# Performance work log

Measured on AMD Instinct MI355X. Metric: run time of the kernel, lower is better.

## Reference

```python
import math
import jax, jax.numpy as jnp
from jax import lax
import numpy as np

E = 16        # num experts
K = 2         # top_k
CF = 1.25     # capacity factor


def setup_inputs() -> dict:
    key = jax.random.key(0)
    k0, k1, k2, k3, k4 = jax.random.split(key, 5)
    B, S, D, H = 2, 2048, 1024, 1024
    scale = 0.02
    return {
        "x": jax.random.normal(k0, (B, S, D), dtype=jnp.float32),
        "router_w": jax.random.normal(k1, (D, E), dtype=jnp.float32) * scale,
        "gate_w": jax.random.normal(k2, (E, D, H), dtype=jnp.float32) * scale,
        "up_w": jax.random.normal(k3, (E, D, H), dtype=jnp.float32) * scale,
        "down_w": jax.random.normal(k4, (E, H, D), dtype=jnp.float32) * scale,
    }


def reference(x, router_w, gate_w, up_w, down_w):
    B, S, D = x.shape
    xf = x.reshape(-1, D)                     # [T, D]
    T = B * S
    capacity = max(1, math.ceil(T * K / E * CF))   # static python int
    Cbuf = K * capacity                       # per-expert buffer (per-column capacity x K)

    # ---- router: softmax over experts, then top-k (weights = top-k probs) ----
    logits = xf @ router_w                    # [T, E]
    probs = jax.nn.softmax(logits, axis=-1)
    w, idx = lax.top_k(probs, K)              # [T, K] each

    # ---- capacity drop: per k-column, per expert, keep first `capacity` tokens ----
    oh = jax.nn.one_hot(idx, E, dtype=w.dtype)            # [T, K, E]
    rank = jnp.cumsum(oh, axis=0) - oh                     # exclusive rank per (k, e)
    myrank = jnp.sum(rank * oh, axis=-1)                   # [T, K]
    keep = myrank < capacity
    w = jnp.where(keep, w, 0.0)

    # ---- dispatch: scatter kept assignments into [E, Cbuf] slots ----
    flat_e = idx.reshape(-1)                               # [A], A = T*K (row-major: token-major)
    flat_w = w.reshape(-1)
    keep_f = keep.reshape(-1)
    tok = jnp.repeat(jnp.arange(T, dtype=jnp.int32), K)    # [A]
    ohk = jax.nn.one_hot(flat_e, E, dtype=jnp.int32) * keep_f[:, None].astype(jnp.int32)
    pos = jnp.cumsum(ohk, axis=0) - ohk                    # exclusive rank among kept per expert
    slot = jnp.sum(pos * ohk, axis=-1)                     # [A], < Cbuf for kept
    e_idx = jnp.where(keep_f, flat_e, E)                   # dropped -> dummy expert row E

    dispatch = jnp.full((E + 1, Cbuf), T, dtype=jnp.int32).at[e_idx, slot].set(tok)
    wbuf = jnp.zeros((E + 1, Cbuf), dtype=w.dtype).at[e_idx, slot].set(flat_w)
    dispatch = dispatch[:E]
    wbuf = wbuf[:E]

    x_pad = jnp.concatenate([xf, jnp.zeros((1, D), xf.dtype)], axis=0)  # sentinel row
    xe = x_pad[dispatch]                                   # [E, Cbuf, D]

    # ---- grouped SwiGLU expert GEMMs ----
    gate = jnp.einsum('ecd,edh->ech', xe, gate_w)
    up = jnp.einsum('ecd,edh->ech', xe, up_w)
    hidden = jax.nn.silu(gate) * up
    out = jnp.einsum('ech,ehd->ecd', hidden, down_w)       # [E, Cbuf, D]
    out = out * wbuf[:, :, None]

    # ---- combine: scatter-add back to tokens ----
    combined = jnp.zeros((T + 1, D), dtype=xf.dtype).at[dispatch.reshape(-1)].add(out.reshape(-1, D))
    return combined[:T].reshape(B, S, D)
```

## Files before the change

kernel.cpp:

```cpp
#include <hip/hip_runtime.h>
#include <math.h>

#define T_TOK 4096
#define DIM   1024
#define HID   1024
#define NE    16
#define CAP   640
#define CBUF  1280
#define BM 128
#define BN 128
#define BK 32
#define MAXTILE 160

typedef __attribute__((ext_vector_type(8))) short short8;
typedef __attribute__((ext_vector_type(4))) float f32x4;

static __device__ __forceinline__ unsigned short f2bf(float f) {
    unsigned int u = __float_as_uint(f);
    u += 0x7fff + ((u >> 16) & 1);
    return (unsigned short)(u >> 16);
}

static __device__ __forceinline__ void async16(const void* g, void* l) {
    __builtin_amdgcn_global_load_lds((const __attribute__((address_space(1))) void*)g,
                                     (__attribute__((address_space(3))) void*)l, 16, 0, 0);
}

__global__ void convert_x_k(const float* __restrict__ x, unsigned short* __restrict__ xb) {
    int i = blockIdx.x * blockDim.x + threadIdx.x;
    int base = i * 4;
    int row = base >> 10;
    ushort4 o;
    if (row < T_TOK) {
        float4 v = *(const float4*)(x + base);
        o.x = f2bf(v.x); o.y = f2bf(v.y); o.z = f2bf(v.z); o.w = f2bf(v.w);
    } else {
        o.x = 0; o.y = 0; o.z = 0; o.w = 0;
    }
    *(ushort4*)(xb + base) = o;
}

#define TSP 68
__global__ void transpose_cvt_k(const float* __restrict__ W0, const float* __restrict__ W1,
                                const float* __restrict__ W2,
                                unsigned short* __restrict__ T0, unsigned short* __restrict__ T1,
                                unsigned short* __restrict__ T2) {
    __shared__ unsigned short s[64 * TSP];
    int zz = blockIdx.z;
    int which = zz >> 4, e = zz & 15;
    const float* W = (which == 0) ? W0 : (which == 1) ? W1 : W2;
    unsigned short* T = (which == 0) ? T0 : (which == 1) ? T1 : T2;
    const float* Wp = W + (size_t)e * DIM * HID;
    unsigned short* Tp = T + (size_t)e * DIM * HID;
    int k0 = blockIdx.y * 64, n0 = blockIdx.x * 64;
    int tid = threadIdx.x;
    int tx = tid & 15, ty = tid >> 4;
    #pragma unroll
    for (int i = 0; i < 4; ++i) {
        int k = ty + i * 16;
        float4 v = *(const float4*)(Wp + (size_t)(k0 + k) * 1024 + n0 + tx * 4);
        int nb = tx * 4;
        s[(nb + 0) * TSP + k] = f2bf(v.x);
        s[(nb + 1) * TSP + k] = f2bf(v.y);
        s[(nb + 2) * TSP + k] = f2bf(v.z);
        s[(nb + 3) * TSP + k] = f2bf(v.w);
    }
    __syncthreads();
    int n = tid >> 2, cseg = (tid & 3) * 16;
    union { ushort4 h[4]; uint4 q[2]; } u;
    #pragma unroll
    for (int j = 0; j < 4; ++j)
        u.h[j] = *(ushort4*)&s[n * TSP + cseg + 4 * j];
    unsigned short* orow = Tp + (size_t)(n0 + n) * 1024 + k0 + cseg;
    *(uint4*)(orow + 0) = u.q[0];
    *(uint4*)(orow + 8) = u.q[1];
}

__global__ void router_k(const float* __restrict__ x, const float* __restrict__ rw,
                         int* __restrict__ route_e, float* __restrict__ route_w) {
    int t = blockIdx.x;
    int lane = threadIdx.x;
    const float* xr = x + (size_t)t * DIM + lane * 16;
    float4 xv0 = *(const float4*)(xr + 0);
    float4 xv1 = *(const float4*)(xr + 4);
    float4 xv2 = *(const float4*)(xr + 8);
    float4 xv3 = *(const float4*)(xr + 12);
    float xl[16] = {xv0.x, xv0.y, xv0.z, xv0.w, xv1.x, xv1.y, xv1.z, xv1.w,
                    xv2.x, xv2.y, xv2.z, xv2.w, xv3.x, xv3.y, xv3.z, xv3.w};
    float p[16];
    #pragma unroll
    for (int e = 0; e < 16; ++e) p[e] = 0.f;
    #pragma unroll
    for (int j = 0; j < 16; ++j) {
        const float4* rp = (const float4*)(rw + (size_t)(lane * 16 + j) * 16);
        float4 r0 = rp[0], r1 = rp[1], r2 = rp[2], r3 = rp[3];
        float xv = xl[j];
        p[0]  += xv * r0.x; p[1]  += xv * r0.y; p[2]  += xv * r0.z; p[3]  += xv * r0.w;
        p[4]  += xv * r1.x; p[5]  += xv * r1.y; p[6]  += xv * r1.z; p[7]  += xv * r1.w;
        p[8]  += xv * r2.x; p[9]  += xv * r2.y; p[10] += xv * r2.z; p[11] += xv * r2.w;
        p[12] += xv * r3.x; p[13] += xv * r3.y; p[14] += xv * r3.z; p[15] += xv * r3.w;
    }
    #pragma unroll
    for (int off = 32; off > 0; off >>= 1) {
        #pragma unroll
        for (int e = 0; e < 16; ++e) p[e] += __shfl_xor(p[e], off);
    }
    if (lane == 0) {
        float m = p[0];
        #pragma unroll
        for (int e = 1; e < 16; ++e) m = fmaxf(m, p[e]);
        float s = 0.f;
        #pragma unroll
        for (int e = 0; e < 16; ++e) s = s + __expf(p[e] - m);
        float v0 = -1e30f, v1 = -1e30f; int i0 = 0, i1 = 0;
        #pragma unroll
        for (int e = 0; e < 16; ++e) {
            float v = p[e];
            if (v > v0)      { v1 = v0; i1 = i0; v0 = v; i0 = e; }
            else if (v > v1) { v1 = v;  i1 = e; }
        }
        route_e[t*2+0] = i0;  route_e[t*2+1] = i1;
        route_w[t*2+0] = __expf(v0 - m) / s;
        route_w[t*2+1] = __expf(v1 - m) / s;
    }
}

__global__ __launch_bounds__(1024)
void build_dispatch_k(const int* __restrict__ route_e, const float* __restrict__ route_w,
                      int* __restrict__ disp, int* __restrict__ smap, int* __restrict__ tmeta) {
    __shared__ unsigned char eidx[2 * T_TOK];
    __shared__ unsigned char keepf[2 * T_TOK];
    __shared__ int totals[NE];
    int tid = threadIdx.x;
    int wv = tid >> 6, lane = tid & 63;

    {
        int4 a = ((const int4*)route_e)[tid * 2];
        int4 b = ((const int4*)route_e)[tid * 2 + 1];
        unsigned int lo = (a.x & 0xff) | ((a.y & 0xff) << 8) | ((a.z & 0xff) << 16) | ((a.w & 0xff) << 24);
        unsigned int hi = (b.x & 0xff) | ((b.y & 0xff) << 8) | ((b.z & 0xff) << 16) | ((b.w & 0xff) << 24);
        uint2 pk; pk.x = lo; pk.y = hi;
        *(uint2*)(eidx + tid * 8) = pk;
    }
    for (int i = tid; i < 2 * T_TOK; i += 1024) smap[i] = -1;
    __syncthreads();

    unsigned long long below = (lane == 0) ? 0ull : ((~0ull) >> (64 - lane));
    #pragma unroll
    for (int s = 0; s < 2; ++s) {
        int st = wv + s * 16;
        int e = st >> 1, k = st & 1;
        int run = 0;
        for (int base = 0; base < T_TOK; base += 64) {
            int t = base + lane;
            int hit = (eidx[t * 2 + k] == e);
            unsigned long long m = __ballot(hit);
            int rank = run + __popcll(m & below);
            if (hit) keepf[t * 2 + k] = (rank < CAP) ? 1 : 0;
            run += __popcll(m);
        }
    }
    __syncthreads();

    {
        int e = wv;
        int run = 0;
        for (int base = 0; base < 2 * T_TOK; base += 64) {
            int f = base + lane;
            int hit = (eidx[f] == e) && keepf[f];
            unsigned long long m = __ballot(hit);
            int slot = run + __popcll(m & below);
            if (hit) {
                disp[e * CBUF + slot] = f >> 1;
                smap[f] = e * CBUF + slot;
            }
            run += __popcll(m);
        }
        if (lane == 0) totals[e] = run;
    }
    __syncthreads();

    for (int i = tid; i < NE * CBUF; i += 1024) {
        int e = i / CBUF, s = i - e * CBUF;
        if (s >= totals[e]) disp[i] = T_TOK;
    }

    if (tid == 0) {
        int n = 0;
        for (int e = 0; e < NE; ++e) {
            int ntl = (totals[e] + BM - 1) / BM;
            for (int m = 0; m < ntl; ++m) { tmeta[4 + n] = (e << 8) | m; ++n; }
        }
        tmeta[0] = n;
    }
}

__global__ __launch_bounds__(256, 2)
void gemm1_k(const unsigned short* __restrict__ xb, const unsigned short* __restrict__ gt,
             const unsigned short* __restrict__ ut, const int* __restrict__ disp,
             const int* __restrict__ tmeta, unsigned short* __restrict__ hidden) {
    int slot = blockIdx.y;
    if (slot >= tmeta[0]) return;
    int pk = tmeta[4 + slot];
    int e = pk >> 8, mt = pk & 255;
    int m0 = mt * BM, n0 = blockIdx.x * BN;

    __shared__ unsigned short As[2 * BM * BK];
    __shared__ unsigned short Bg[2 * BN * BK];
    __shared__ unsigned short Bu[2 * BN * BK];
    __shared__ int tok[BM];
    int tid = threadIdx.x;
    if (tid < BM) tok[tid] = disp[e * CBUF + m0 + tid];
    __syncthreads();

    int lane = tid & 63, w = tid >> 6;
    int cg = (lane & 3) ^ ((lane >> 3) & 3);
    int rl = lane >> 2;
    int rA0 = w * 32 + rl, rA1 = rA0 + 16;
    const unsigned short* srcA0 = xb + (size_t)tok[rA0] * DIM + cg * 8;
    const unsigned short* srcA1 = xb + (size_t)tok[rA1] * DIM + cg * 8;
    const unsigned short* srcG0 = gt + ((size_t)e * HID + n0 + rA0) * DIM + cg * 8;
    const unsigned short* srcG1 = gt + ((size_t)e * HID + n0 + rA1) * DIM + cg * 8;
    const unsigned short* srcU0 = ut + ((size_t)e * HID + n0 + rA0) * DIM + cg * 8;
    const unsigned short* srcU1 = ut + ((size_t)e * HID + n0 + rA1) * DIM + cg * 8;
    unsigned short* dA0 = As + (w * 32) * BK;
    unsigned short* dA1 = As + (w * 32 + 16) * BK;
    unsigned short* dG0 = Bg + (w * 32) * BK;
    unsigned short* dG1 = Bg + (w * 32 + 16) * BK;
    unsigned short* dU0 = Bu + (w * 32) * BK;
    unsigned short* dU1 = Bu + (w * 32 + 16) * BK;

    int wm = w >> 1, wn = w & 1;
    int quad = lane >> 4, ln = lane & 15;
    int swq = quad ^ ((ln >> 1) & 3);

    f32x4 zero4 = {0.f, 0.f, 0.f, 0.f};
    f32x4 accg[4][4], accu[4][4];
    #pragma unroll
    for (int i = 0; i < 4; ++i)
        #pragma unroll
        for (int j = 0; j < 4; ++j) { accg[i][j] = zero4; accu[i][j] = zero4; }

    async16(srcA0, dA0); async16(srcA1, dA1);
    async16(srcG0, dG0); async16(srcG1, dG1);
    async16(srcU0, dU0); async16(srcU1, dU1);

    for (int k0 = 0; k0 < DIM; k0 += BK) {
        int cur = (k0 >> 5) & 1;
        asm volatile("s_waitcnt vmcnt(0)\n\ts_barrier" ::: "memory");
        if (k0 + BK < DIM) {
            int nx = cur ^ 1, nk = k0 + BK;
            async16(srcA0 + nk, dA0 + nx * (BM * BK));
            async16(srcA1 + nk, dA1 + nx * (BM * BK));
            async16(srcG0 + nk, dG0 + nx * (BN * BK));
            async16(srcG1 + nk, dG1 + nx * (BN * BK));
            async16(srcU0 + nk, dU0 + nx * (BN * BK));
            async16(srcU1 + nk, dU1 + nx * (BN * BK));
        }
        const unsigned short* Ab = As + cur * (BM * BK);
        const unsigned short* Gb = Bg + cur * (BN * BK);
        const unsigned short* Ub = Bu + cur * (BN * BK);
        short8 af[4], bgf[4], buf2[4];
        #pragma unroll
        for (int i = 0; i < 4; ++i)
            af[i] = *(const short8*)(Ab + (wm * 64 + i * 16 + ln) * BK + swq * 8);
        #pragma unroll
        for (int j = 0; j < 4; ++j) {
            bgf[j]  = *(const short8*)(Gb + (wn * 64 + j * 16 + ln) * BK + swq * 8);
            buf2[j] = *(const short8*)(Ub + (wn * 64 + j * 16 + ln) * BK + swq * 8);
        }
        #pragma unroll
        for (int i = 0; i < 4; ++i)
            #pragma unroll
            for (int j = 0; j < 4; ++j) {
                accg[i][j] = __builtin_amdgcn_mfma_f32_16x16x32_bf16(af[i], bgf[j],  accg[i][j], 0, 0, 0);
                accu[i][j] = __builtin_amdgcn_mfma_f32_16x16x32_bf16(af[i], buf2[j], accu[i][j], 0, 0, 0);
            }
    }
    #pragma unroll
    for (int i = 0; i < 4; ++i) {
        #pragma unroll
        for (int r = 0; r < 4; ++r) {
            int row = m0 + wm * 64 + i * 16 + quad * 4 + r;
            unsigned short* hrow = hidden + ((size_t)e * CBUF + row) * HID + n0 + wn * 64 + ln;
            #pragma unroll
            for (int j = 0; j < 4; ++j) {
                float g = accg[i][j][r];
                float u = accu[i][j][r];
                float sg = g / (1.f + __expf(-g));
                hrow[j * 16] = f2bf(sg * u);
            }
        }
    }
}

__global__ __launch_bounds__(256, 2)
void gemm2_k(const unsigned short* __restrict__ hidden, const unsigned short* __restrict__ dt,
             const int* __restrict__ tmeta, unsigned short* __restrict__ ebuf) {
    int slot = blockIdx.y;
    if (slot >= tmeta[0]) return;
    int pk = tmeta[4 + slot];
    int e = pk >> 8, mt = pk & 255;
    int m0 = mt * BM, n0 = blockIdx.x * BN;

    __shared__ unsigned short As[2 * BM * BK];
    __shared__ unsigned short Bs[2 * BN * BK];
    int tid = threadIdx.x;

    int lane = tid & 63, w = tid >> 6;
    int cg = (lane & 3) ^ ((lane >> 3) & 3);
    int rl = lane >> 2;
    int rA0 = w * 32 + rl, rA1 = rA0 + 16;
    const unsigned short* srcA0 = hidden + ((size_t)e * CBUF + m0 + rA0) * HID + cg * 8;
    const unsigned short* srcA1 = hidden + ((size_t)e * CBUF + m0 + rA1) * HID + cg * 8;
    const unsigned short* srcB0 = dt + ((size_t)e * DIM + n0 + rA0) * HID + cg * 8;
    const unsigned short* srcB1 = dt + ((size_t)e * DIM + n0 + rA1) * HID + cg * 8;
    unsigned short* dA0 = As + (w * 32) * BK;
    unsigned short* dA1 = As + (w * 32 + 16) * BK;
    unsigned short* dB0 = Bs + (w * 32) * BK;
    unsigned short* dB1 = Bs + (w * 32 + 16) * BK;

    int wm = w >> 1, wn = w & 1;
    int quad = lane >> 4, ln = lane & 15;
    int swq = quad ^ ((ln >> 1) & 3);

    f32x4 zero4 = {0.f, 0.f, 0.f, 0.f};
    f32x4 acc[4][4];
    #pragma unroll
    for (int i = 0; i < 4; ++i)
        #pragma unroll
        for (int j = 0; j < 4; ++j) acc[i][j] = zero4;

    async16(srcA0, dA0); async16(srcA1, dA1);
    async16(srcB0, dB0); async16(srcB1, dB1);

    for (int k0 = 0; k0 < HID; k0 += BK) {
        int cur = (k0 >> 5) & 1;
        asm volatile("s_waitcnt vmcnt(0)\n\ts_barrier" ::: "memory");
        if (k0 + BK < HID) {
            int nx = cur ^ 1, nk = k0 + BK;
            async16(srcA0 + nk, dA0 + nx * (BM * BK));
            async16(srcA1 + nk, dA1 + nx * (BM * BK));
            async16(srcB0 + nk, dB0 + nx * (BN * BK));
            async16(srcB1 + nk, dB1 + nx * (BN * BK));
        }
        const unsigned short* Ab = As + cur * (BM * BK);
        const unsigned short* Bb = Bs + cur * (BN * BK);
        short8 af[4], bf[4];
        #pragma unroll
        for (int i = 0; i < 4; ++i)
            af[i] = *(const short8*)(Ab + (wm * 64 + i * 16 + ln) * BK + swq * 8);
        #pragma unroll
        for (int j = 0; j < 4; ++j)
            bf[j] = *(const short8*)(Bb + (wn * 64 + j * 16 + ln) * BK + swq * 8);
        #pragma unroll
        for (int i = 0; i < 4; ++i)
            #pragma unroll
            for (int j = 0; j < 4; ++j)
                acc[i][j] = __builtin_amdgcn_mfma_f32_16x16x32_bf16(af[i], bf[j], acc[i][j], 0, 0, 0);
    }
    #pragma unroll
    for (int i = 0; i < 4; ++i) {
        #pragma unroll
        for (int r = 0; r < 4; ++r) {
            int row = m0 + wm * 64 + i * 16 + quad * 4 + r;
            unsigned short* erow = ebuf + ((size_t)e * CBUF + row) * DIM + n0 + wn * 64 + ln;
            #pragma unroll
            for (int j = 0; j < 4; ++j)
                erow[j * 16] = f2bf(acc[i][j][r]);
        }
    }
}

__global__ __launch_bounds__(256)
void combine_k(const unsigned short* __restrict__ ebuf, const int* __restrict__ smap,
               const float* __restrict__ rwt, float* __restrict__ out) {
    int t = blockIdx.x * 2 + (threadIdx.x >> 7);
    int c = (threadIdx.x & 127) * 8;
    float acc[8];
    #pragma unroll
    for (int j = 0; j < 8; ++j) acc[j] = 0.f;
    #pragma unroll
    for (int k = 0; k < 2; ++k) {
        int sm = smap[t * 2 + k];
        if (sm >= 0) {
            float wgt = rwt[t * 2 + k];
            uint4 rv = *(const uint4*)(ebuf + (size_t)sm * DIM + c);
            unsigned int d[4] = {rv.x, rv.y, rv.z, rv.w};
            #pragma unroll
            for (int q = 0; q < 4; ++q) {
                acc[q * 2 + 0] += wgt * __uint_as_float(d[q] << 16);
                acc[q * 2 + 1] += wgt * __uint_as_float(d[q] & 0xffff0000u);
            }
        }
    }
    float4 o0 = {acc[0], acc[1], acc[2], acc[3]};
    float4 o1 = {acc[4], acc[5], acc[6], acc[7]};
    float* orow = out + (size_t)t * DIM + c;
    *(float4*)(orow + 0) = o0;
    *(float4*)(orow + 4) = o1;
}

extern "C" void kernel_launch(void* const* d_in, const int* in_sizes, int n_in,
                              void* d_out, int out_size, void* d_ws, size_t ws_size,
                              hipStream_t stream) {
    const float* x  = (const float*)d_in[0];
    const float* rw = (const float*)d_in[1];
    const float* gw = (const float*)d_in[2];
    const float* uw = (const float*)d_in[3];
    const float* dw = (const float*)d_in[4];
    float* out = (float*)d_out;

    char* ws = (char*)d_ws;
    size_t off = 0;
    auto alloc = [&](size_t bytes) { void* p = ws + off; off += (bytes + 255) & ~(size_t)255; return p; };
    unsigned short* xb  = (unsigned short*)alloc((size_t)(T_TOK + 1) * DIM * 2);
    unsigned short* gt  = (unsigned short*)alloc((size_t)NE * DIM * HID * 2);
    unsigned short* ut  = (unsigned short*)alloc((size_t)NE * DIM * HID * 2);
    unsigned short* dtw = (unsigned short*)alloc((size_t)NE * DIM * HID * 2);
    unsigned short* hid = (unsigned short*)alloc((size_t)NE * CBUF * HID * 2);
    int*   disp   = (int*)alloc((size_t)NE * CBUF * 4);
    int*   smap   = (int*)alloc((size_t)T_TOK * 2 * 4);
    int*   tmeta  = (int*)alloc((4 + MAXTILE) * 4);
    int*   re     = (int*)alloc((size_t)T_TOK * 2 * 4);
    float* rwt    = (float*)alloc((size_t)T_TOK * 2 * 4);
    unsigned short* ebuf = gt;
    (void)ws_size; (void)in_sizes; (void)n_in;

    convert_x_k<<<T_TOK + 1, 256, 0, stream>>>(x, xb);
    transpose_cvt_k<<<dim3(16, 16, 48), 256, 0, stream>>>(gw, uw, dw, gt, ut, dtw);
    router_k<<<T_TOK, 64, 0, stream>>>(x, rw, re, rwt);
    build_dispatch_k<<<1, 1024, 0, stream>>>(re, rwt, disp, smap, tmeta);
    gemm1_k<<<dim3(HID / BN, MAXTILE), 256, 0, stream>>>(xb, gt, ut, disp, tmeta, hid);
    gemm2_k<<<dim3(DIM / BN, MAXTILE), 256, 0, stream>>>(hid, dtw, tmeta, ebuf);
    combine_k<<<T_TOK / 2, 256, 0, stream>>>(ebuf, smap, rwt, out);
}
```

Before: 413.1 us.

## Triple-buffer gemm2 async LDS loads and rework weight transpose store pattern

Converts the down-projection GEMM's async global-to-LDS pipeline from double to triple buffering. It prefetches two K-tiles ahead and waits only for the older batch (vmcnt(4)), so memory latency overlaps more with the MFMA work. The weight transpose kernel also changes its LDS padding and readout so each thread writes one 16-byte chunk per row, which is meant to cut bank conflicts. Extra LDS per block may lower occupancy relative to launch_bounds(256,2).

```diff
diff --git a/kernel.cpp b/kernel.cpp
--- a/kernel.cpp
+++ b/kernel.cpp
@@ -40,7 +40,7 @@
     *(ushort4*)(xb + base) = o;
 }
 
-#define TSP 68
+#define TSP 66
 __global__ void transpose_cvt_k(const float* __restrict__ W0, const float* __restrict__ W1,
                                 const float* __restrict__ W2,
                                 unsigned short* __restrict__ T0, unsigned short* __restrict__ T1,
@@ -66,14 +66,18 @@
         s[(nb + 3) * TSP + k] = f2bf(v.w);
     }
     __syncthreads();
-    int n = tid >> 2, cseg = (tid & 3) * 16;
-    union { ushort4 h[4]; uint4 q[2]; } u;
-    #pragma unroll
-    for (int j = 0; j < 4; ++j)
-        u.h[j] = *(ushort4*)&s[n * TSP + cseg + 4 * j];
-    unsigned short* orow = Tp + (size_t)(n0 + n) * 1024 + k0 + cseg;
-    *(uint4*)(orow + 0) = u.q[0];
-    *(uint4*)(orow + 8) = u.q[1];
+    int j = tid & 7, kseg = j * 8;
+    int nb2 = tid >> 3;
+    #pragma unroll
+    for (int h = 0; h < 2; ++h) {
+        int n = h * 32 + nb2;
+        uint4 o;
+        o.x = *(const unsigned int*)&s[n * TSP + kseg + 0];
+        o.y = *(const unsigned int*)&s[n * TSP + kseg + 2];
+        o.z = *(const unsigned int*)&s[n * TSP + kseg + 4];
+        o.w = *(const unsigned int*)&s[n * TSP + kseg + 6];
+        *(uint4*)(Tp + (size_t)(n0 + n) * 1024 + k0 + kseg) = o;
+    }
 }
 
 __global__ void router_k(const float* __restrict__ x, const float* __restrict__ rw,
@@ -303,8 +307,8 @@
     int e = pk >> 8, mt = pk & 255;
     int m0 = mt * BM, n0 = blockIdx.x * BN;
 
-    __shared__ unsigned short As[2 * BM * BK];
-    __shared__ unsigned short Bs[2 * BN * BK];
+    __shared__ unsigned short As[3 * BM * BK];
+    __shared__ unsigned short Bs[3 * BN * BK];
     int tid = threadIdx.x;
 
     int lane = tid & 63, w = tid >> 6;
@@ -333,19 +337,25 @@
 
     async16(srcA0, dA0); async16(srcA1, dA1);
     async16(srcB0, dB0); async16(srcB1, dB1);
+    async16(srcA0 + BK, dA0 + BM * BK); async16(srcA1 + BK, dA1 + BM * BK);
+    async16(srcB0 + BK, dB0 + BN * BK); async16(srcB1 + BK, dB1 + BN * BK);
 
     for (int k0 = 0; k0 < HID; k0 += BK) {
-        int cur = (k0 >> 5) & 1;
-        asm volatile("s_waitcnt vmcnt(0)\n\ts_barrier" ::: "memory");
+        int stage = (k0 >> 5) % 3;
         if (k0 + BK < HID) {
-            int nx = cur ^ 1, nk = k0 + BK;
+            asm volatile("s_waitcnt vmcnt(4)\n\ts_barrier" ::: "memory");
+        } else {
+            asm volatile("s_waitcnt vmcnt(0)\n\ts_barrier" ::: "memory");
+        }
+        if (k0 + 2 * BK < HID) {
+            int nx = (stage + 2) % 3, nk = k0 + 2 * BK;
             async16(srcA0 + nk, dA0 + nx * (BM * BK));
             async16(srcA1 + nk, dA1 + nx * (BM * BK));
             async16(srcB0 + nk, dB0 + nx * (BN * BK));
             async16(srcB1 + nk, dB1 + nx * (BN * BK));
         }
-        const unsigned short* Ab = As + cur * (BM * BK);
-        const unsigned short* Bb = Bs + cur * (BN * BK);
+        const unsigned short* Ab = As + stage * (BM * BK);
+        const unsigned short* Bb = Bs + stage * (BN * BK);
         short8 af[4], bf[4];
         #pragma unroll
         for (int i = 0; i < 4; ++i)
```

Measured after the change: 415.1 us. About the same (+0.5%).
